# Performance work log

Hardware: AMD Instinct MI355X
Metric: run time of the kernel (lower is better)

The kernel has to match this reference:

```python
import jax, jax.numpy as jnp
import numpy as np

PATCH = 3
ALPHA = 0.5
EPS = 1e-12  # F.normalize default eps


def _unfold(x, p):
    # nn.Unfold(kernel_size=p, padding=p//2) then reshape(B, C, p*p, H*W)
    B, C, H, W = x.shape
    pad = p // 2
    xp = jnp.pad(x, ((0, 0), (0, 0), (pad, pad), (pad, pad)))
    # kernel positions row-major, matching torch unfold channel-major layout
    pats = jnp.stack([xp[:, :, i:i + H, j:j + W]
                      for i in range(p) for j in range(p)], axis=2)  # [B,C,K,H,W]
    return pats.reshape(B, C, p * p, H * W)


def setup_inputs() -> dict:
    key = jax.random.key(0)
    k1, k2 = jax.random.split(key)
    B, C, H, W = 4, 32, 256, 256
    fe_lv = jax.random.normal(k1, (B, C, H, W), dtype=jnp.float32)
    fused_features = jax.random.normal(k2, (B, C, H, W), dtype=jnp.float32)
    return {"fe_lv": fe_lv, "fused_features": fused_features}


def reference(fe_lv, fused_features):
    B, C, H, W = fe_lv.shape
    N = H * W
    patches = _unfold(fused_features, PATCH)          # [B,C,K,N]
    fe_flat = fe_lv.reshape(B, C, N)                  # [B,C,N]

    # cosine similarity over channel dim
    pn = patches / jnp.maximum(jnp.linalg.norm(patches, axis=1, keepdims=True), EPS)
    fn = fe_flat / jnp.maximum(jnp.linalg.norm(fe_flat, axis=1, keepdims=True), EPS)
    cosine_sim = jnp.einsum('bckn,bcn->bnk', pn, fn)  # [B,N,K]
    cosine_weights = jax.nn.softmax(cosine_sim, axis=-1)

    # euclidean distance over channel dim
    dist = jnp.sqrt(jnp.sum((patches - fe_flat[:, :, None, :]) ** 2, axis=1))  # [B,K,N]
    euclidean_weights = jax.nn.softmax(-dist.transpose(0, 2, 1), axis=-1)      # [B,N,K]

    weights = ALPHA * cosine_weights + (1.0 - ALPHA) * euclidean_weights
    refined = jnp.einsum('bnk,bckn->bcn', weights, patches)  # [B,C,N]
    return refined.reshape(B, C, H, W) + fe_lv
```

## Files before the change

kernel.cpp:

```cpp
#include <hip/hip_runtime.h>
#include <math.h>

#define B_ 4
#define C_ 32
#define H_ 256
#define W_ 256
#define HW_ (H_ * W_)
#define K_ 9
#define TX 32
#define TY 8
#define HX 34
#define HY 10
#define HCH (HX * HY)
#define NPX (TX * TY)
#define NOCT 4
#define FUH8 (NOCT * HCH)
#define FEH8 (NOCT * NPX)
#define EPS_ 1e-12f

typedef _Float16 h2v __attribute__((ext_vector_type(2)));
typedef _Float16 h8v __attribute__((ext_vector_type(8)));

#if defined(__has_builtin)
#if __has_builtin(__builtin_amdgcn_fdot2)
#define HAVE_FDOT2 1
#endif
#if __has_builtin(__builtin_amdgcn_cvt_pkrtz)
#define HAVE_PKRTZ 1
#endif
#endif

static __device__ __forceinline__ h2v pk2(float a, float b) {
#if defined(HAVE_PKRTZ)
    return __builtin_bit_cast(h2v, __builtin_amdgcn_cvt_pkrtz(a, b));
#else
    h2v r = {(_Float16)a, (_Float16)b};
    return r;
#endif
}

static __device__ __forceinline__ float dot2(h2v a, h2v b, float c) {
#if defined(HAVE_FDOT2)
    return __builtin_amdgcn_fdot2(a, b, c, false);
#else
    return c + (float)a[0] * (float)b[0] + (float)a[1] * (float)b[1];
#endif
}

__global__ __launch_bounds__(512, 4) void asfr_kernel(const float* __restrict__ fe,
                                                      const float* __restrict__ fu,
                                                      float* __restrict__ out) {
    __shared__ h8v lds8[FUH8 + FEH8];
    const int t = threadIdx.x;
    const int bx = blockIdx.x & 7;
    const int by = (blockIdx.x >> 3) & 31;
    const int b  = blockIdx.x >> 8;
    const int w0 = bx * TX, h0 = by * TY;

    const float* fub = fu + b * (C_ * HW_);
    const float* feb = fe + b * (C_ * HW_);

#pragma unroll
    for (int j = 0; j < 3; ++j) {
        int u = t + j * 512;
        if (u < FUH8) {
            int oct = u / HCH;
            int pos = u - oct * HCH;
            int r = pos / HX;
            int col = pos - r * HX;
            int hh = h0 - 1 + r;
            int ww = w0 - 1 + col;
            bool ok = ((unsigned)hh < (unsigned)H_) && ((unsigned)ww < (unsigned)W_);
            int hcl = hh < 0 ? 0 : (hh > H_ - 1 ? H_ - 1 : hh);
            int wcl = ww < 0 ? 0 : (ww > W_ - 1 ? W_ - 1 : ww);
            const float* gp = fub + (oct * 8) * HW_ + hcl * W_ + wcl;
            float v[8];
#pragma unroll
            for (int c = 0; c < 8; ++c) v[c] = gp[c * HW_];
            float m = ok ? 1.f : 0.f;
#pragma unroll
            for (int c = 0; c < 8; ++c) v[c] *= m;
            h8v hv;
#pragma unroll
            for (int c = 0; c < 4; ++c) {
                h2v p = pk2(v[2 * c], v[2 * c + 1]);
                hv[2 * c] = p[0];
                hv[2 * c + 1] = p[1];
            }
            lds8[oct * HCH + pos] = hv;
        }
    }

#pragma unroll
    for (int j = 0; j < 2; ++j) {
        int u = t + j * 512;
        int oct = u >> 8;
        int px = u & (NPX - 1);
        int hh = h0 + (px >> 5);
        int ww = w0 + (px & 31);
        const float* gp = feb + (oct * 8) * HW_ + hh * W_ + ww;
        float v[8];
#pragma unroll
        for (int c = 0; c < 8; ++c) v[c] = gp[c * HW_];
        h8v hv;
#pragma unroll
        for (int c = 0; c < 4; ++c) {
            h2v p = pk2(v[2 * c], v[2 * c + 1]);
            hv[2 * c] = p[0];
            hv[2 * c + 1] = p[1];
        }
        lds8[FUH8 + oct * NPX + px] = hv;
    }
    __syncthreads();

    const int x = t & 31;
    const int half = (t >> 5) & 1;
    const int y = t >> 6;
    const int pxl = (y << 5) + x;
    const int pxoff = b * (C_ * HW_) + (h0 + y) * W_ + (w0 + x);
    const int hc = (y + 1) * HX + (x + 1);
    const int koff[K_] = {-HX - 1, -HX, -HX + 1, -1, 0, 1, HX - 1, HX, HX + 1};

    float dot[K_], psq[K_];
#pragma unroll
    for (int k = 0; k < K_; ++k) { dot[k] = 0.f; psq[k] = 0.f; }
    float fsq = 0.f;

#pragma unroll
    for (int j = 0; j < 2; ++j) {
        const int oct = 2 * half + j;
        h8v fq = lds8[FUH8 + oct * NPX + pxl];
        h2v fA0 = __builtin_shufflevector(fq, fq, 0, 1);
        h2v fA1 = __builtin_shufflevector(fq, fq, 2, 3);
        h2v fA2 = __builtin_shufflevector(fq, fq, 4, 5);
        h2v fA3 = __builtin_shufflevector(fq, fq, 6, 7);
        fsq = dot2(fA0, fA0, fsq);
        fsq = dot2(fA1, fA1, fsq);
        fsq = dot2(fA2, fA2, fsq);
        fsq = dot2(fA3, fA3, fsq);
        const h8v* fubase = &lds8[oct * HCH + hc];
#pragma unroll
        for (int k = 0; k < K_; ++k) {
            h8v p8 = fubase[koff[k]];
            h2v p0 = __builtin_shufflevector(p8, p8, 0, 1);
            h2v p1 = __builtin_shufflevector(p8, p8, 2, 3);
            h2v p2 = __builtin_shufflevector(p8, p8, 4, 5);
            h2v p3 = __builtin_shufflevector(p8, p8, 6, 7);
            dot[k] = dot2(p0, fA0, dot[k]);
            dot[k] = dot2(p1, fA1, dot[k]);
            dot[k] = dot2(p2, fA2, dot[k]);
            dot[k] = dot2(p3, fA3, dot[k]);
            psq[k] = dot2(p0, p0, psq[k]);
            psq[k] = dot2(p1, p1, psq[k]);
            psq[k] = dot2(p2, p2, psq[k]);
            psq[k] = dot2(p3, p3, psq[k]);
        }
    }

#pragma unroll
    for (int k = 0; k < K_; ++k) {
        dot[k] += __shfl_xor(dot[k], 32);
        psq[k] += __shfl_xor(psq[k], 32);
    }
    fsq += __shfl_xor(fsq, 32);

    float nf = fmaxf(sqrtf(fsq), EPS_);
    float cosv[K_], negd[K_];
#pragma unroll
    for (int k = 0; k < K_; ++k) {
        float np = fmaxf(sqrtf(psq[k]), EPS_);
        cosv[k] = __fdividef(dot[k], np * nf);
        float dsq = fmaxf(psq[k] - 2.f * dot[k] + fsq, 0.f);
        negd[k] = -sqrtf(dsq);
    }

    float m1 = cosv[0], m2 = negd[0];
#pragma unroll
    for (int k = 1; k < K_; ++k) { m1 = fmaxf(m1, cosv[k]); m2 = fmaxf(m2, negd[k]); }
    float s1 = 0.f, s2 = 0.f, e1[K_], e2[K_];
#pragma unroll
    for (int k = 0; k < K_; ++k) {
        e1[k] = __expf(cosv[k] - m1);
        e2[k] = __expf(negd[k] - m2);
        s1 += e1[k]; s2 += e2[k];
    }
    float r1 = __fdividef(0.5f, s1), r2 = __fdividef(0.5f, s2);
    h2v w2[K_];
#pragma unroll
    for (int k = 0; k < K_; ++k) {
        float wk = fmaf(e1[k], r1, e2[k] * r2);
        _Float16 wh = (_Float16)wk;
        h2v tmp = {wh, wh};
        w2[k] = tmp;
    }

#pragma unroll
    for (int j = 0; j < 2; ++j) {
        const int oct = 2 * half + j;
        const h8v* fubase = &lds8[oct * HCH + hc];
        h2v a0 = {(_Float16)0, (_Float16)0};
        h2v a1 = a0, a2 = a0, a3 = a0;
#pragma unroll
        for (int k = 0; k < K_; ++k) {
            h8v p8 = fubase[koff[k]];
            a0 += w2[k] * __builtin_shufflevector(p8, p8, 0, 1);
            a1 += w2[k] * __builtin_shufflevector(p8, p8, 2, 3);
            a2 += w2[k] * __builtin_shufflevector(p8, p8, 4, 5);
            a3 += w2[k] * __builtin_shufflevector(p8, p8, 6, 7);
        }
        h8v fq = lds8[FUH8 + oct * NPX + pxl];
        const int cg = oct * 8;
        out[pxoff + (cg + 0) * HW_] = (float)(fq[0] + a0[0]);
        out[pxoff + (cg + 1) * HW_] = (float)(fq[1] + a0[1]);
        out[pxoff + (cg + 2) * HW_] = (float)(fq[2] + a1[0]);
        out[pxoff + (cg + 3) * HW_] = (float)(fq[3] + a1[1]);
        out[pxoff + (cg + 4) * HW_] = (float)(fq[4] + a2[0]);
        out[pxoff + (cg + 5) * HW_] = (float)(fq[5] + a2[1]);
        out[pxoff + (cg + 6) * HW_] = (float)(fq[6] + a3[0]);
        out[pxoff + (cg + 7) * HW_] = (float)(fq[7] + a3[1]);
    }
}

extern "C" void kernel_launch(void* const* d_in, const int* in_sizes, int n_in,
                              void* d_out, int out_size, void* d_ws, size_t ws_size,
                              hipStream_t stream) {
    const float* fe = (const float*)d_in[0];
    const float* fu = (const float*)d_in[1];
    float* out = (float*)d_out;
    dim3 grid((W_ / TX) * (H_ / TY) * B_), block(512);
    hipLaunchKernelGGL(asfr_kernel, grid, block, 0, stream, fe, fu, out);
}
```

Before: 35.12 us.

## Halve tile height and load fe directly into registers instead of LDS

The tile shrinks from 32x8 to 32x4 pixels, the block from 512 to 256 threads, and the grid doubles. Each thread now loads its 16 fe channels straight from global memory into registers and packs them to half precision, so the fe staging area in shared memory and its reload are gone. The aim is to cut LDS footprint, allow more resident blocks, and shorten the path for fe. The cost is a larger halo ratio: 6 rows are loaded per 4 output rows instead of 10 per 8, which means more redundant global reads of fu.

```diff
diff --git a/kernel.cpp b/kernel.cpp
--- a/kernel.cpp
+++ b/kernel.cpp
@@ -8,14 +8,12 @@
 #define HW_ (H_ * W_)
 #define K_ 9
 #define TX 32
-#define TY 8
+#define TY 4
 #define HX 34
-#define HY 10
+#define HY 6
 #define HCH (HX * HY)
-#define NPX (TX * TY)
 #define NOCT 4
 #define FUH8 (NOCT * HCH)
-#define FEH8 (NOCT * NPX)
 #define EPS_ 1e-12f
 
 typedef _Float16 h2v __attribute__((ext_vector_type(2)));
@@ -47,61 +45,46 @@
 #endif
 }
 
-__global__ __launch_bounds__(512, 4) void asfr_kernel(const float* __restrict__ fe,
+__global__ __launch_bounds__(256, 8) void asfr_kernel(const float* __restrict__ fe,
                                                       const float* __restrict__ fu,
                                                       float* __restrict__ out) {
-    __shared__ h8v lds8[FUH8 + FEH8];
+    __shared__ h8v lds8[FUH8];
     const int t = threadIdx.x;
     const int bx = blockIdx.x & 7;
-    const int by = (blockIdx.x >> 3) & 31;
-    const int b  = blockIdx.x >> 8;
+    const int by = (blockIdx.x >> 3) & 63;
+    const int b  = blockIdx.x >> 9;
     const int w0 = bx * TX, h0 = by * TY;
 
+    const int x = t & 31;
+    const int half = (t >> 5) & 1;
+    const int y = t >> 6;
+    const int c0 = half << 4;
+    const int pxoff = b * (C_ * HW_) + (h0 + y) * W_ + (w0 + x);
+
+    float fv[16];
+#pragma unroll
+    for (int cc = 0; cc < 16; ++cc) fv[cc] = fe[pxoff + (c0 + cc) * HW_];
+
     const float* fub = fu + b * (C_ * HW_);
-    const float* feb = fe + b * (C_ * HW_);
-
 #pragma unroll
     for (int j = 0; j < 3; ++j) {
-        int u = t + j * 512;
-        if (u < FUH8) {
-            int oct = u / HCH;
-            int pos = u - oct * HCH;
-            int r = pos / HX;
-            int col = pos - r * HX;
-            int hh = h0 - 1 + r;
-            int ww = w0 - 1 + col;
-            bool ok = ((unsigned)hh < (unsigned)H_) && ((unsigned)ww < (unsigned)W_);
-            int hcl = hh < 0 ? 0 : (hh > H_ - 1 ? H_ - 1 : hh);
-            int wcl = ww < 0 ? 0 : (ww > W_ - 1 ? W_ - 1 : ww);
-            const float* gp = fub + (oct * 8) * HW_ + hcl * W_ + wcl;
-            float v[8];
-#pragma unroll
-            for (int c = 0; c < 8; ++c) v[c] = gp[c * HW_];
-            float m = ok ? 1.f : 0.f;
-#pragma unroll
-            for (int c = 0; c < 8; ++c) v[c] *= m;
-            h8v hv;
-#pragma unroll
-            for (int c = 0; c < 4; ++c) {
-                h2v p = pk2(v[2 * c], v[2 * c + 1]);
-                hv[2 * c] = p[0];
-                hv[2 * c + 1] = p[1];
-            }
-            lds8[oct * HCH + pos] = hv;
-        }
-    }
-
-#pragma unroll
-    for (int j = 0; j < 2; ++j) {
-        int u = t + j * 512;
-        int oct = u >> 8;
-        int px = u & (NPX - 1);
-        int hh = h0 + (px >> 5);
-        int ww = w0 + (px & 31);
-        const float* gp = feb + (oct * 8) * HW_ + hh * W_ + ww;
+        int u = t + j * 256;
+        int oct = u / HCH;
+        int pos = u - oct * HCH;
+        int r = pos / HX;
+        int col = pos - r * HX;
+        int hh = h0 - 1 + r;
+        int ww = w0 - 1 + col;
+        bool ok = ((unsigned)hh < (unsigned)H_) && ((unsigned)ww < (unsigned)W_);
+        int hcl = hh < 0 ? 0 : (hh > H_ - 1 ? H_ - 1 : hh);
+        int wcl = ww < 0 ? 0 : (ww > W_ - 1 ? W_ - 1 : ww);
+        const float* gp = fub + (oct * 8) * HW_ + hcl * W_ + wcl;
         float v[8];
 #pragma unroll
         for (int c = 0; c < 8; ++c) v[c] = gp[c * HW_];
+        float m = ok ? 1.f : 0.f;
+#pragma unroll
+        for (int c = 0; c < 8; ++c) v[c] *= m;
         h8v hv;
 #pragma unroll
         for (int c = 0; c < 4; ++c) {
@@ -109,15 +92,48 @@
             hv[2 * c] = p[0];
             hv[2 * c + 1] = p[1];
         }
-        lds8[FUH8 + oct * NPX + px] = hv;
+        lds8[u] = hv;
+    }
+    if (t < FUH8 - 768) {
+        int u = t + 768;
+        int oct = u / HCH;
+        int pos = u - oct * HCH;
+        int r = pos / HX;
+        int col = pos - r * HX;
+        int hh = h0 - 1 + r;
+        int ww = w0 - 1 + col;
+        bool ok = ((unsigned)hh < (unsigned)H_) && ((unsigned)ww < (unsigned)W_);
+        int hcl = hh < 0 ? 0 : (hh > H_ - 1 ? H_ - 1 : hh);
+        int wcl = ww < 0 ? 0 : (ww > W_ - 1 ? W_ - 1 : ww);
+        const float* gp = fub + (oct * 8) * HW_ + hcl * W_ + wcl;
+        float v[8];
+#pragma unroll
+        for (int c = 0; c < 8; ++c) v[c] = gp[c * HW_];
+        float m = ok ? 1.f : 0.f;
+#pragma unroll
+        for (int c = 0; c < 8; ++c) v[c] *= m;
+        h8v hv;
+#pragma unroll
+        for (int c = 0; c < 4; ++c) {
+            h2v p = pk2(v[2 * c], v[2 * c + 1]);
+            hv[2 * c] = p[0];
+            hv[2 * c + 1] = p[1];
+        }
+        lds8[u] = hv;
+    }
+
+    h8v fe8[2];
+#pragma unroll
+    for (int j = 0; j < 2; ++j) {
+#pragma unroll
+        for (int c = 0; c < 4; ++c) {
+            h2v p = pk2(fv[8 * j + 2 * c], fv[8 * j + 2 * c + 1]);
+            fe8[j][2 * c] = p[0];
+            fe8[j][2 * c + 1] = p[1];
+        }
     }
     __syncthreads();
 
-    const int x = t & 31;
-    const int half = (t >> 5) & 1;
-    const int y = t >> 6;
-    const int pxl = (y << 5) + x;
-    const int pxoff = b * (C_ * HW_) + (h0 + y) * W_ + (w0 + x);
     const int hc = (y + 1) * HX + (x + 1);
     const int koff[K_] = {-HX - 1, -HX, -HX + 1, -1, 0, 1, HX - 1, HX, HX + 1};
 
@@ -129,7 +145,7 @@
 #pragma unroll
     for (int j = 0; j < 2; ++j) {
         const int oct = 2 * half + j;
-        h8v fq = lds8[FUH8 + oct * NPX + pxl];
+        h8v fq = fe8[j];
         h2v fA0 = __builtin_shufflevector(fq, fq, 0, 1);
         h2v fA1 = __builtin_shufflevector(fq, fq, 2, 3);
         h2v fA2 = __builtin_shufflevector(fq, fq, 4, 5);
@@ -208,7 +224,7 @@
             a2 += w2[k] * __builtin_shufflevector(p8, p8, 4, 5);
             a3 += w2[k] * __builtin_shufflevector(p8, p8, 6, 7);
         }
-        h8v fq = lds8[FUH8 + oct * NPX + pxl];
+        h8v fq = fe8[j];
         const int cg = oct * 8;
         out[pxoff + (cg + 0) * HW_] = (float)(fq[0] + a0[0]);
         out[pxoff + (cg + 1) * HW_] = (float)(fq[1] + a0[1]);
@@ -227,6 +243,6 @@
     const float* fe = (const float*)d_in[0];
     const float* fu = (const float*)d_in[1];
     float* out = (float*)d_out;
-    dim3 grid((W_ / TX) * (H_ / TY) * B_), block(512);
+    dim3 grid((W_ / TX) * (H_ / TY) * B_), block(256);
     hipLaunchKernelGGL(asfr_kernel, grid, block, 0, stream, fe, fu, out);
 }
```

New measurement: 44.05 us. 1.25x slower.
